# Kernel tuning notes

Hardware: AMD Instinct MI355X
Metric: run time of the kernel (lower is better)

## Reference

```python
import jax, jax.numpy as jnp
import numpy as np

EPS = 1e-7
OBJ_W, CLS_W, BOX_W = 1.5, 1.5, 0.5
NEG_OBJ_W, POS_OBJ_W = 0.5, 1.5


def setup_inputs() -> dict:
    key = jax.random.key(0)
    k1, k2 = jax.random.split(key)
    B, N, C = 32, 19200, 80
    outputs = jax.random.uniform(k1, (B, N, 5 + C), dtype=jnp.float32)
    targets = jax.random.uniform(k2, (B, N, 5 + C), dtype=jnp.float32)
    return {"outputs": outputs, "targets": targets}


def _xyxy(box):
    # (cx, cy, w, h) -> (x1, y1, x2, y2)
    cx, cy, w, h = box[..., 0], box[..., 1], box[..., 2], box[..., 3]
    return cx - w / 2, cy - h / 2, cx + w / 2, cy + h / 2


def _focal(logits, tgt, alpha, gamma):
    # torchvision.ops.sigmoid_focal_loss (reduction='none')
    p = jax.nn.sigmoid(logits)
    ce = jnp.maximum(logits, 0) - logits * tgt + jnp.log1p(jnp.exp(-jnp.abs(logits)))
    p_t = p * tgt + (1 - p) * (1 - tgt)
    loss = ce * (1 - p_t) ** gamma
    alpha_t = alpha * tgt + (1 - alpha) * (1 - tgt)
    return alpha_t * loss


def _ciou_loss(pred, gt):
    # torchvision.ops.complete_box_iou_loss, boxes in cxcywh
    px1, py1, px2, py2 = _xyxy(pred)
    gx1, gy1, gx2, gy2 = _xyxy(gt)
    iw = jnp.clip(jnp.minimum(px2, gx2) - jnp.maximum(px1, gx1), 0)
    ih = jnp.clip(jnp.minimum(py2, gy2) - jnp.maximum(py1, gy1), 0)
    inter = iw * ih
    union = (px2 - px1) * (py2 - py1) + (gx2 - gx1) * (gy2 - gy1) - inter
    iou = inter / (union + EPS)
    # enclosing box diagonal
    cw = jnp.maximum(px2, gx2) - jnp.minimum(px1, gx1)
    ch = jnp.maximum(py2, gy2) - jnp.minimum(py1, gy1)
    diag = cw * cw + ch * ch + EPS
    dist = ((px1 + px2 - gx1 - gx2) ** 2 + (py1 + py2 - gy1 - gy2) ** 2) / 4
    # aspect-ratio term
    w_p, h_p = px2 - px1, py2 - py1
    w_g, h_g = gx2 - gx1, gy2 - gy1
    v = (4 / (jnp.pi ** 2)) * (jnp.arctan(w_g / (h_g + EPS)) - jnp.arctan(w_p / (h_p + EPS))) ** 2
    a = jax.lax.stop_gradient(v / (1 - iou + v + EPS))
    return 1 - iou + dist / diag + a * v


def _loss(outputs, targets):
    # channels: [cx, cy, w, h, conf, classes...]
    pred_box, pred_conf, pred_cls = outputs[..., :4], outputs[..., 4], outputs[..., 5:]
    gt_box, gt_conf, gt_cls = targets[..., :4], targets[..., 4], targets[..., 5:]
    N = outputs.shape[1]

    pos = gt_conf > 0.5                      # [B, N] grid cells with a GT (conf_threshold=0.5)
    posf = pos.astype(outputs.dtype)

    ciou = _ciou_loss(pred_box, gt_box)      # [B, N]
    # matched cells: cls focal (alpha=0.5, gamma=0), mean over classes
    cls_l = _focal(pred_cls, gt_cls, 0.5, 0.0).mean(-1)
    # matched cells: positive objectness vs target 1 (alpha clamps to 0.5 with 1 pred/cell)
    pos_obj = _focal(pred_conf, jnp.ones_like(pred_conf), 0.5, 0.0) * POS_OBJ_W
    # unmatched cells: negative objectness vs target 0 (alpha=0.5, gamma=1.5)
    neg_obj = _focal(pred_conf, jnp.zeros_like(pred_conf), 0.5, 1.5) * NEG_OBJ_W
    obj = jnp.where(pos, pos_obj, neg_obj)

    # per-image mean over all grid cells (negatives contribute 0 ciou/cls)
    ciou_img = (ciou * posf).sum(1) / N
    cls_img = (cls_l * posf).sum(1) / N
    obj_img = obj.mean(1)
    n_pos = jnp.maximum(posf.sum(1), 1.0)
    pos_obj_img = (pos_obj * posf).sum(1) / n_pos

    avg_ciou = ciou_img.mean()
    avg_obj = obj_img.mean()
    avg_cls = cls_img.mean()
    avg_pos_obj = pos_obj_img.mean()
    total = BOX_W * avg_ciou + OBJ_W * avg_obj + CLS_W * avg_cls
    return (total, avg_ciou * BOX_W, avg_obj * OBJ_W, avg_cls * CLS_W, avg_pos_obj)


def reference(outputs, targets):
    return _loss(outputs, targets)
```

## Files before the change

### kernel.cpp

```cpp
#include <hip/hip_runtime.h>
#include <math.h>

constexpr int B  = 32;
constexpr int N  = 19200;
constexpr int CH = 85;
constexpr float EPSF = 1e-7f;

constexpr int THREADS   = 256;
constexpr int TILE_A    = 16;
constexpr int TILE_F    = TILE_A * CH;
constexpr int TILE_F4   = TILE_F / 4;
constexpr int STAGE_F4  = 2 * TILE_F4;
constexpr int STAGE_PAD = 768;
constexpr int Qn        = THREADS / TILE_A;
constexpr int CLS_PER_Q = 80 / Qn;

constexpr int TILES_PER_IMG   = N / TILE_A;
constexpr int BLOCKS_PER_IMG  = 48;
constexpr int BLOCKS          = B * BLOCKS_PER_IMG;
constexpr int TILES_PER_BLOCK = TILES_PER_IMG / BLOCKS_PER_IMG;


__device__ __forceinline__ float bce(float l, float t) {
    float sp = __logf(1.0f + __expf(-fabsf(l)));
    return fmaxf(l, 0.0f) - l * t + sp;
}

__global__ __launch_bounds__(THREADS) void loss_main(
    const float4* __restrict__ go4, const float4* __restrict__ gt4,
    float* __restrict__ ws) {

    __shared__ float4 buf[2][STAGE_PAD];
    __shared__ float  red[THREADS / 64][5];

    const int tid  = threadIdx.x;
    const int lane = tid & 63;
    const int wav  = tid >> 6;

    const int bimg  = blockIdx.x / BLOCKS_PER_IMG;
    const int tile0 = bimg * TILES_PER_IMG
                    + (blockIdx.x % BLOCKS_PER_IMG) * TILES_PER_BLOCK;

    const int a = tid >> 4;
    const int q = tid & 15;

    float v0 = 0.0f, v1 = 0.0f, v2 = 0.0f, v3 = 0.0f, v4 = 0.0f;

    auto stage = [&](int bsel, int tile) {
        const float4* gob = go4 + (size_t)tile * TILE_F4;
        const float4* gtb = gt4 + (size_t)tile * TILE_F4;
        #pragma unroll
        for (int k = 0; k < 3; ++k) {
            const int i  = wav * 64 + k * 256 + lane;
            const int ic = (i < STAGE_F4) ? i : (STAGE_F4 - 1);
            const float4* src = (ic >= TILE_F4) ? (gtb + (ic - TILE_F4)) : (gob + ic);
            float4* dst = &buf[bsel][wav * 64 + k * 256];
            __builtin_amdgcn_global_load_lds(
                (const __attribute__((address_space(1))) void*)src,
                (__attribute__((address_space(3))) void*)dst, 16, 0, 0);
        }
    };

    stage(0, tile0);
    int cur = 0;

    for (int t = 0; t < TILES_PER_BLOCK; ++t) {
        if (t + 1 < TILES_PER_BLOCK) {
            stage(cur ^ 1, tile0 + t + 1);
            asm volatile("s_waitcnt vmcnt(3)" ::: "memory");
        } else {
            asm volatile("s_waitcnt vmcnt(0)" ::: "memory");
        }
        __builtin_amdgcn_s_barrier();

        const float* bf = (const float*)&buf[cur][0];

        {
            const float* lo = bf + a * CH;
            const float* lt = bf + TILE_F + a * CH;
            const float posf = (lt[4] > 0.5f) ? 1.0f : 0.0f;

            float s = 0.0f;
            const int c0 = 5 + CLS_PER_Q * q;
            #pragma unroll
            for (int j = 0; j < CLS_PER_Q; ++j) {
                s += bce(lo[c0 + j], lt[c0 + j]);
            }
            v1 += posf * s;
        }

        if (wav == (t & 3) && lane < TILE_A) {
            const float* lo = bf + lane * CH;
            const float* lt = bf + TILE_F + lane * CH;

            const float gconf = lt[4];
            const float posf  = (gconf > 0.5f) ? 1.0f : 0.0f;

            const float o = lo[4];
            float pos_obj = 0.75f * bce(o, 1.0f);
            float p       = 1.0f / (1.0f + __expf(-o));
            float neg_obj = 0.25f * bce(o, 0.0f) * p * sqrtf(p);
            v2 += (posf > 0.0f) ? pos_obj : neg_obj;
            v3 += posf;
            v4 += pos_obj * posf;

            float pcx = lo[0], pcy = lo[1], pw = lo[2], ph = lo[3];
            float gcx = lt[0], gcy = lt[1], gw = lt[2], gh = lt[3];

            float px1 = pcx - pw * 0.5f, px2 = pcx + pw * 0.5f;
            float py1 = pcy - ph * 0.5f, py2 = pcy + ph * 0.5f;
            float gx1 = gcx - gw * 0.5f, gx2 = gcx + gw * 0.5f;
            float gy1 = gcy - gh * 0.5f, gy2 = gcy + gh * 0.5f;

            float iwd   = fmaxf(fminf(px2, gx2) - fmaxf(px1, gx1), 0.0f);
            float ihd   = fmaxf(fminf(py2, gy2) - fmaxf(py1, gy1), 0.0f);
            float inter = iwd * ihd;
            float uni   = (px2 - px1) * (py2 - py1) + (gx2 - gx1) * (gy2 - gy1) - inter;
            float iou   = inter / (uni + EPSF);

            float cw   = fmaxf(px2, gx2) - fminf(px1, gx1);
            float chh  = fmaxf(py2, gy2) - fminf(py1, gy1);
            float diag = cw * cw + chh * chh + EPSF;
            float dx   = px1 + px2 - gx1 - gx2;
            float dy   = py1 + py2 - gy1 - gy2;
            float dist = (dx * dx + dy * dy) * 0.25f;

            float w_p = px2 - px1, h_p = py2 - py1;
            float w_g = gx2 - gx1, h_g = gy2 - gy1;
            float datan = atanf(w_g / (h_g + EPSF)) - atanf(w_p / (h_p + EPSF));
            const float four_over_pi2 = 4.0f / (float)(M_PI * M_PI);
            float vv = four_over_pi2 * datan * datan;
            float aa = vv / (1.0f - iou + vv + EPSF);
            float ciou = 1.0f - iou + dist / diag + aa * vv;

            v0 += ciou * posf;
        }

        __builtin_amdgcn_s_barrier();
        cur ^= 1;
    }

    v1 *= 0.5f * (1.0f / 80.0f);

    #pragma unroll
    for (int off = 32; off > 0; off >>= 1) {
        v0 += __shfl_down(v0, off);
        v1 += __shfl_down(v1, off);
        v2 += __shfl_down(v2, off);
        v3 += __shfl_down(v3, off);
        v4 += __shfl_down(v4, off);
    }

    if (lane == 0) {
        red[wav][0] = v0; red[wav][1] = v1; red[wav][2] = v2;
        red[wav][3] = v3; red[wav][4] = v4;
    }
    __syncthreads();

    if (tid == 0) {
        float s0 = 0, s1 = 0, s2 = 0, s3 = 0, s4 = 0;
        #pragma unroll
        for (int w = 0; w < THREADS / 64; ++w) {
            s0 += red[w][0]; s1 += red[w][1]; s2 += red[w][2];
            s3 += red[w][3]; s4 += red[w][4];
        }
        float* slot = ws + (size_t)blockIdx.x * 8;
        slot[0] = s0; slot[1] = s1; slot[2] = s2; slot[3] = s3; slot[4] = s4;
    }
}

__global__ void loss_final(const float* __restrict__ ws, float* __restrict__ out) {
    const int j = threadIdx.x;
    constexpr int SLOTS_PER_T = BLOCKS / 64;

    double s0 = 0, s1 = 0, s2 = 0, s3 = 0, s4 = 0;
    for (int k = 0; k < SLOTS_PER_T; ++k) {
        const float* p = ws + (size_t)(j * SLOTS_PER_T + k) * 8;
        s0 += p[0]; s1 += p[1]; s2 += p[2]; s3 += p[3]; s4 += p[4];
    }

    double n3 = s3 + __shfl_xor(s3, 1);
    double n4 = s4 + __shfl_xor(s4, 1);
    double npos = (n3 < 1.0) ? 1.0 : n3;
    double pim  = ((j & 1) == 0) ? (n4 / npos) : 0.0;

    #pragma unroll
    for (int off = 32; off > 0; off >>= 1) {
        s0  += __shfl_down(s0, off);
        s1  += __shfl_down(s1, off);
        s2  += __shfl_down(s2, off);
        pim += __shfl_down(pim, off);
    }

    if (j == 0) {
        const double inv = 1.0 / ((double)N * (double)B);
        double avg_ciou   = s0 * inv;
        double avg_cls    = s1 * inv;
        double avg_obj    = s2 * inv;
        double avg_posobj = pim / (double)B;

        double t1 = 0.5 * avg_ciou;
        double t2 = 1.5 * avg_obj;
        double t3 = 1.5 * avg_cls;
        out[0] = (float)(t1 + t2 + t3);
        out[1] = (float)t1;
        out[2] = (float)t2;
        out[3] = (float)t3;
        out[4] = (float)avg_posobj;
    }
}

extern "C" void kernel_launch(void* const* d_in, const int* in_sizes, int n_in,
                              void* d_out, int out_size, void* d_ws, size_t ws_size,
                              hipStream_t stream) {
    const float* outputs = (const float*)d_in[0];
    const float* targets = (const float*)d_in[1];

    loss_main<<<BLOCKS, THREADS, 0, stream>>>(
        (const float4*)outputs, (const float4*)targets, (float*)d_ws);
    loss_final<<<1, 64, 0, stream>>>((const float*)d_ws, (float*)d_out);
}
```

Before: 88.78 us.

## Batch box/objectness work across four tiles via LDS stash to fill wavefront lanes

Per-anchor CIoU and objectness math previously ran on only 16 lanes of one wavefront per tile. The first three of every four tiles now stash their 10 box/conf fields in shared memory, and the fourth tile has one wave compute all 64 anchors at full lane occupancy. Leftover tiles are handled after the loop. Global source pointers are also precomputed and incremented instead of recomputed each stage. This adds LDS writes and a shared stash, plus tail handling that relies on the tile count per block.

New measurement: 86.71 us. 2.3% less time.

```diff
diff --git a/kernel.cpp b/kernel.cpp
--- a/kernel.cpp
+++ b/kernel.cpp
@@ -26,11 +26,55 @@
     return fmaxf(l, 0.0f) - l * t + sp;
 }
 
+__device__ __forceinline__ void obj_ciou(
+    float pcx, float pcy, float pw, float ph, float pconf,
+    float gcx, float gcy, float gw, float gh, float gconf,
+    float& v0, float& v2, float& v3, float& v4) {
+
+    const float posf = (gconf > 0.5f) ? 1.0f : 0.0f;
+
+    float pos_obj = 0.75f * bce(pconf, 1.0f);
+    float p       = 1.0f / (1.0f + __expf(-pconf));
+    float neg_obj = 0.25f * bce(pconf, 0.0f) * p * sqrtf(p);
+    v2 += (posf > 0.0f) ? pos_obj : neg_obj;
+    v3 += posf;
+    v4 += pos_obj * posf;
+
+    float px1 = pcx - pw * 0.5f, px2 = pcx + pw * 0.5f;
+    float py1 = pcy - ph * 0.5f, py2 = pcy + ph * 0.5f;
+    float gx1 = gcx - gw * 0.5f, gx2 = gcx + gw * 0.5f;
+    float gy1 = gcy - gh * 0.5f, gy2 = gcy + gh * 0.5f;
+
+    float iwd   = fmaxf(fminf(px2, gx2) - fmaxf(px1, gx1), 0.0f);
+    float ihd   = fmaxf(fminf(py2, gy2) - fmaxf(py1, gy1), 0.0f);
+    float inter = iwd * ihd;
+    float uni   = (px2 - px1) * (py2 - py1) + (gx2 - gx1) * (gy2 - gy1) - inter;
+    float iou   = inter / (uni + EPSF);
+
+    float cw   = fmaxf(px2, gx2) - fminf(px1, gx1);
+    float chh  = fmaxf(py2, gy2) - fminf(py1, gy1);
+    float diag = cw * cw + chh * chh + EPSF;
+    float dx   = px1 + px2 - gx1 - gx2;
+    float dy   = py1 + py2 - gy1 - gy2;
+    float dist = (dx * dx + dy * dy) * 0.25f;
+
+    float w_p = px2 - px1, h_p = py2 - py1;
+    float w_g = gx2 - gx1, h_g = gy2 - gy1;
+    float datan = atanf(w_g / (h_g + EPSF)) - atanf(w_p / (h_p + EPSF));
+    const float four_over_pi2 = 4.0f / (float)(M_PI * M_PI);
+    float vv = four_over_pi2 * datan * datan;
+    float aa = vv / (1.0f - iou + vv + EPSF);
+    float ciou = 1.0f - iou + dist / diag + aa * vv;
+
+    v0 += ciou * posf;
+}
+
 __global__ __launch_bounds__(THREADS) void loss_main(
     const float4* __restrict__ go4, const float4* __restrict__ gt4,
     float* __restrict__ ws) {
 
     __shared__ float4 buf[2][STAGE_PAD];
+    __shared__ float  stash[3][TILE_A][11];
     __shared__ float  red[THREADS / 64][5];
 
     const int tid  = threadIdx.x;
@@ -44,29 +88,41 @@
     const int a = tid >> 4;
     const int q = tid & 15;
 
+    const int sa = tid / 10;
+    const int sf = tid - sa * 10;
+    const int stash_src_off = sa * CH + ((sf < 5) ? sf : (TILE_F + sf - 5));
+
     float v0 = 0.0f, v1 = 0.0f, v2 = 0.0f, v3 = 0.0f, v4 = 0.0f;
 
-    auto stage = [&](int bsel, int tile) {
-        const float4* gob = go4 + (size_t)tile * TILE_F4;
-        const float4* gtb = gt4 + (size_t)tile * TILE_F4;
+    const float4* src[3];
+    {
+        const float4* gob = go4 + (size_t)tile0 * TILE_F4;
+        const float4* gtb = gt4 + (size_t)tile0 * TILE_F4;
         #pragma unroll
         for (int k = 0; k < 3; ++k) {
             const int i  = wav * 64 + k * 256 + lane;
             const int ic = (i < STAGE_F4) ? i : (STAGE_F4 - 1);
-            const float4* src = (ic >= TILE_F4) ? (gtb + (ic - TILE_F4)) : (gob + ic);
+            src[k] = (ic >= TILE_F4) ? (gtb + (ic - TILE_F4)) : (gob + ic);
+        }
+    }
+
+    auto stage = [&](int bsel) {
+        #pragma unroll
+        for (int k = 0; k < 3; ++k) {
             float4* dst = &buf[bsel][wav * 64 + k * 256];
             __builtin_amdgcn_global_load_lds(
-                (const __attribute__((address_space(1))) void*)src,
+                (const __attribute__((address_space(1))) void*)src[k],
                 (__attribute__((address_space(3))) void*)dst, 16, 0, 0);
+            src[k] += TILE_F4;
         }
     };
 
-    stage(0, tile0);
+    stage(0);
     int cur = 0;
 
     for (int t = 0; t < TILES_PER_BLOCK; ++t) {
         if (t + 1 < TILES_PER_BLOCK) {
-            stage(cur ^ 1, tile0 + t + 1);
+            stage(cur ^ 1);
             asm volatile("s_waitcnt vmcnt(3)" ::: "memory");
         } else {
             asm volatile("s_waitcnt vmcnt(0)" ::: "memory");
@@ -89,55 +145,35 @@
             v1 += posf * s;
         }
 
-        if (wav == (t & 3) && lane < TILE_A) {
-            const float* lo = bf + lane * CH;
-            const float* lt = bf + TILE_F + lane * CH;
-
-            const float gconf = lt[4];
-            const float posf  = (gconf > 0.5f) ? 1.0f : 0.0f;
-
-            const float o = lo[4];
-            float pos_obj = 0.75f * bce(o, 1.0f);
-            float p       = 1.0f / (1.0f + __expf(-o));
-            float neg_obj = 0.25f * bce(o, 0.0f) * p * sqrtf(p);
-            v2 += (posf > 0.0f) ? pos_obj : neg_obj;
-            v3 += posf;
-            v4 += pos_obj * posf;
-
-            float pcx = lo[0], pcy = lo[1], pw = lo[2], ph = lo[3];
-            float gcx = lt[0], gcy = lt[1], gw = lt[2], gh = lt[3];
-
-            float px1 = pcx - pw * 0.5f, px2 = pcx + pw * 0.5f;
-            float py1 = pcy - ph * 0.5f, py2 = pcy + ph * 0.5f;
-            float gx1 = gcx - gw * 0.5f, gx2 = gcx + gw * 0.5f;
-            float gy1 = gcy - gh * 0.5f, gy2 = gcy + gh * 0.5f;
-
-            float iwd   = fmaxf(fminf(px2, gx2) - fmaxf(px1, gx1), 0.0f);
-            float ihd   = fmaxf(fminf(py2, gy2) - fmaxf(py1, gy1), 0.0f);
-            float inter = iwd * ihd;
-            float uni   = (px2 - px1) * (py2 - py1) + (gx2 - gx1) * (gy2 - gy1) - inter;
-            float iou   = inter / (uni + EPSF);
-
-            float cw   = fmaxf(px2, gx2) - fminf(px1, gx1);
-            float chh  = fmaxf(py2, gy2) - fminf(py1, gy1);
-            float diag = cw * cw + chh * chh + EPSF;
-            float dx   = px1 + px2 - gx1 - gx2;
-            float dy   = py1 + py2 - gy1 - gy2;
-            float dist = (dx * dx + dy * dy) * 0.25f;
-
-            float w_p = px2 - px1, h_p = py2 - py1;
-            float w_g = gx2 - gx1, h_g = gy2 - gy1;
-            float datan = atanf(w_g / (h_g + EPSF)) - atanf(w_p / (h_p + EPSF));
-            const float four_over_pi2 = 4.0f / (float)(M_PI * M_PI);
-            float vv = four_over_pi2 * datan * datan;
-            float aa = vv / (1.0f - iou + vv + EPSF);
-            float ciou = 1.0f - iou + dist / diag + aa * vv;
-
-            v0 += ciou * posf;
+        if ((t & 3) != 3 && tid < 160) {
+            stash[t & 3][sa][sf] = bf[stash_src_off];
+        }
+
+        if ((t & 3) == 3 && wav == ((t >> 2) & 3)) {
+            float o0,o1,o2,o3,o4, g0,g1,g2,g3,g4;
+            if (lane < 48) {
+                const float* sp = &stash[lane >> 4][lane & 15][0];
+                o0=sp[0]; o1=sp[1]; o2=sp[2]; o3=sp[3]; o4=sp[4];
+                g0=sp[5]; g1=sp[6]; g2=sp[7]; g3=sp[8]; g4=sp[9];
+            } else {
+                const float* lo = bf + (lane - 48) * CH;
+                const float* lt = bf + TILE_F + (lane - 48) * CH;
+                o0=lo[0]; o1=lo[1]; o2=lo[2]; o3=lo[3]; o4=lo[4];
+                g0=lt[0]; g1=lt[1]; g2=lt[2]; g3=lt[3]; g4=lt[4];
+            }
+            obj_ciou(o0,o1,o2,o3,o4, g0,g1,g2,g3,g4, v0, v2, v3, v4);
         }
 
         __builtin_amdgcn_s_barrier();
         cur ^= 1;
+    }
+
+    if (wav == 2 && lane < TILE_A) {
+        const float* bfL = (const float*)&buf[cur ^ 1][0];
+        const float* lo = bfL + lane * CH;
+        const float* lt = bfL + TILE_F + lane * CH;
+        obj_ciou(lo[0],lo[1],lo[2],lo[3],lo[4],
+                 lt[0],lt[1],lt[2],lt[3],lt[4], v0, v2, v3, v4);
     }
 
     v1 *= 0.5f * (1.0f / 80.0f);
```
